# Performance work log

Hardware: AMD Instinct MI355X
Metric: run time of the kernel (lower is better)

Reference implementation:

```python
import jax, jax.numpy as jnp
import numpy as np

TEMP = 0.1        # Similarity temperature (nonzero -> cosine path)
PAD = -100.0      # padding value used by the torch module
EPS = 1e-8        # F.cosine_similarity default eps


def setup_inputs() -> dict:
    key = jax.random.key(0)
    k1, k2, k3 = jax.random.split(key, 3)
    B, S, D = 8, 4096, 1024
    sequence_output = jax.random.normal(k1, (B, S, D), dtype=jnp.float32)
    cls = jax.random.randint(k2, (B, S), 0, 2, dtype=jnp.int32)
    is_eop = jax.random.uniform(k3, (B, S)) < 0.25
    labels = jnp.where(is_eop, cls, -100).astype(jnp.int32)
    return {"sequence_output": sequence_output, "labels": labels}


def reference(sequence_output, labels):
    # sequence_output: [B, S, D]; labels: [B, S] with -100 = ignore
    B, S, D = sequence_output.shape
    mask = labels != -100                      # [B, S]
    cnt = mask.sum(axis=1)                     # [B] eop sentence count per example
    # Stable argsort brings masked (eop) positions to the front, preserving order
    order = jnp.argsort(jnp.logical_not(mask), axis=1, stable=True)  # [B, S]
    gathered = jnp.take_along_axis(sequence_output, order[..., None], axis=1)  # [B, S, D]
    glabels = jnp.take_along_axis(labels, order, axis=1)                        # [B, S]

    pos = jnp.arange(S)[None, :]               # [1, S]
    cnt_safe = jnp.maximum(cnt, 1)[:, None]    # avoid %0 for empty examples
    nxt = (pos + 1) % cnt_safe                 # [B, S] cyclic next-sentence index
    next_vec = jnp.take_along_axis(gathered, nxt[..., None], axis=1)  # [B, S, D]

    dot = jnp.sum(gathered * next_vec, axis=-1)                 # [B, S]
    nx = jnp.linalg.norm(gathered, axis=-1)
    ny = jnp.linalg.norm(next_vec, axis=-1)
    cos = dot / jnp.maximum(nx * ny, EPS) / TEMP                # cosine / temp

    valid = pos < cnt[:, None]                                  # [B, S]
    # Torch pads to the max eop count in the batch; we pad to S (static upper
    # bound) with the same -100 fill so the math on valid slots is identical.
    cos_out = jnp.where(valid, cos, PAD)
    lab_out = jnp.where(valid, glabels, -100)
    return cos_out, lab_out
```

## Files before the change

### kernel.cpp

```cpp
#include <hip/hip_runtime.h>

#define BB 8
#define SS 4096
#define DD 1024
#define TEMP 0.1f
#define PADV -100.0f
#define EPSV 1e-8f

__global__ __launch_bounds__(1024) void compact_kernel(const int* __restrict__ labels,
                                                       int2* __restrict__ desc,
                                                       float* __restrict__ out_cos,
                                                       float* __restrict__ out_lab) {
    int b = blockIdx.x;
    int t = threadIdx.x;
    int lane = t & 63, wave = t >> 6;

    __shared__ int pos[SS];
    __shared__ int wsum[16];

    int4 v = ((const int4*)(labels + b * SS))[t];
    int vals[4] = {v.x, v.y, v.z, v.w};
    int mycnt = (vals[0] != -100) + (vals[1] != -100) + (vals[2] != -100) + (vals[3] != -100);

    int scan = mycnt;
#pragma unroll
    for (int off = 1; off < 64; off <<= 1) {
        int n = __shfl_up(scan, off, 64);
        if (lane >= off) scan += n;
    }
    if (lane == 63) wsum[wave] = scan;
    __syncthreads();

    int wbase = 0, c = 0;
#pragma unroll
    for (int w = 0; w < 16; ++w) {
        int s = wsum[w];
        wbase += (w < wave) ? s : 0;
        c += s;
    }
    int o = wbase + scan - mycnt;

#pragma unroll
    for (int i = 0; i < 4; ++i) {
        if (vals[i] != -100) {
            pos[o]              = 4 * t + i;
            out_lab[b * SS + o] = (float)vals[i];
            ++o;
        }
    }
#pragma unroll
    for (int i = 0; i < 4; ++i) {
        int s = 4 * t + i;
        if (s >= c) { out_lab[b * SS + s] = PADV; out_cos[b * SS + s] = PADV; }
    }
    __syncthreads();

    int2 d[4];
#pragma unroll
    for (int i = 0; i < 4; ++i) {
        int j = 4 * t + i;
        if (j < c) {
            int jn = (j + 1 == c) ? 0 : (j + 1);
            d[i].x = pos[j];
            d[i].y = pos[jn];
        } else {
            d[i].x = -1;
            d[i].y = -1;
        }
    }
    int4* dp = (int4*)(desc + (size_t)b * SS + 4 * t);
    dp[0] = make_int4(d[0].x, d[0].y, d[1].x, d[1].y);
    dp[1] = make_int4(d[2].x, d[2].y, d[3].x, d[3].y);
}

__global__ __launch_bounds__(256) void cos_kernel(const float* __restrict__ x,
                                                  const int2* __restrict__ desc,
                                                  float* __restrict__ out_cos) {
    int b    = blockIdx.y;
    int lane = threadIdx.x & 63;
    int wid  = threadIdx.x >> 6;
    int j0   = (blockIdx.x * 4 + wid) * 2;

    int4 D = *(const int4*)(desc + (size_t)b * SS + j0);
    if (D.x < 0) return;
    bool p1 = (D.z >= 0);
    int i0 = D.x, i1 = D.y;
    int i2 = p1 ? D.w : D.y;

    const float* xb = x + (size_t)b * SS * DD + (size_t)lane * 4;
    const float* pa = xb + (size_t)i0 * DD;
    const float* pb = xb + (size_t)i1 * DD;
    const float* pc = xb + (size_t)i2 * DD;

    float4 A[4], B[4], C[4];
#pragma unroll
    for (int q = 0; q < 4; ++q) {
        A[q] = *(const float4*)(pa + q * 256);
        B[q] = *(const float4*)(pb + q * 256);
        C[q] = *(const float4*)(pc + q * 256);
    }

    float na = 0.f, nb = 0.f, nc = 0.f, dab = 0.f, dbc = 0.f;
#pragma unroll
    for (int q = 0; q < 4; ++q) {
        na  += A[q].x*A[q].x + A[q].y*A[q].y + A[q].z*A[q].z + A[q].w*A[q].w;
        nb  += B[q].x*B[q].x + B[q].y*B[q].y + B[q].z*B[q].z + B[q].w*B[q].w;
        nc  += C[q].x*C[q].x + C[q].y*C[q].y + C[q].z*C[q].z + C[q].w*C[q].w;
        dab += A[q].x*B[q].x + A[q].y*B[q].y + A[q].z*B[q].z + A[q].w*B[q].w;
        dbc += B[q].x*C[q].x + B[q].y*C[q].y + B[q].z*C[q].z + B[q].w*C[q].w;
    }
#pragma unroll
    for (int off = 32; off; off >>= 1) {
        na  += __shfl_xor(na,  off, 64);
        nb  += __shfl_xor(nb,  off, 64);
        nc  += __shfl_xor(nc,  off, 64);
        dab += __shfl_xor(dab, off, 64);
        dbc += __shfl_xor(dbc, off, 64);
    }

    if (lane == 0) {
        float r0 = dab / fmaxf(sqrtf(na) * sqrtf(nb), EPSV) / TEMP;
        float* op = out_cos + b * SS + j0;
        if (p1) {
            float r1 = dbc / fmaxf(sqrtf(nb) * sqrtf(nc), EPSV) / TEMP;
            *(float2*)op = make_float2(r0, r1);
        } else {
            *op = r0;
        }
    }
}

extern "C" void kernel_launch(void* const* d_in, const int* in_sizes, int n_in,
                              void* d_out, int out_size, void* d_ws, size_t ws_size,
                              hipStream_t stream) {
    const float* seq    = (const float*)d_in[0];
    const int*   labels = (const int*)d_in[1];

    float* out_cos = (float*)d_out;
    float* out_lab = (float*)d_out + BB * SS;

    int2* desc = (int2*)d_ws;

    compact_kernel<<<BB, 1024, 0, stream>>>(labels, desc, out_cos, out_lab);

    dim3 grid(SS / 8, BB);
    cos_kernel<<<grid, 256, 0, stream>>>(seq, desc, out_cos);
}
```

Baseline: 16.51 us.

## Stage shared row vectors in LDS via direct global-to-LDS loads per block

Each block now handles 8 consecutive compacted positions and loads the 9 distinct rows they need into shared memory once, using the direct global_load_lds builtin. Waves then read their three rows from LDS instead of reloading overlapping rows from global memory. This removes the duplicate fetch of the boundary row shared by adjacent waves (12 row loads per block down to 9). In exchange it adds a block-wide barrier, 36KB of LDS per block that limits occupancy, and an extra LDS round trip.

Result: slower. 17.38 us (+5.3%).

```diff
diff --git a/kernel.cpp b/kernel.cpp
--- a/kernel.cpp
+++ b/kernel.cpp
@@ -6,6 +6,9 @@
 #define TEMP 0.1f
 #define PADV -100.0f
 #define EPSV 1e-8f
+
+typedef __attribute__((address_space(1))) const void GV;
+typedef __attribute__((address_space(3))) void LV;
 
 __global__ __launch_bounds__(1024) void compact_kernel(const int* __restrict__ labels,
                                                        int2* __restrict__ desc,
@@ -77,27 +80,60 @@
                                                   const int2* __restrict__ desc,
                                                   float* __restrict__ out_cos) {
     int b    = blockIdx.y;
-    int lane = threadIdx.x & 63;
-    int wid  = threadIdx.x >> 6;
-    int j0   = (blockIdx.x * 4 + wid) * 2;
+    int j0   = blockIdx.x * 8;
+    int t    = threadIdx.x;
+    int lane = t & 63, wid = t >> 6;
 
-    int4 D = *(const int4*)(desc + (size_t)b * SS + j0);
-    if (D.x < 0) return;
-    bool p1 = (D.z >= 0);
-    int i0 = D.x, i1 = D.y;
-    int i2 = p1 ? D.w : D.y;
+    __shared__ float buf[9 * 1024];
 
-    const float* xb = x + (size_t)b * SS * DD + (size_t)lane * 4;
-    const float* pa = xb + (size_t)i0 * DD;
-    const float* pb = xb + (size_t)i1 * DD;
-    const float* pc = xb + (size_t)i2 * DD;
+    const int2* dbase = desc + (size_t)b * SS + j0;
+    int4 d01 = *(const int4*)(dbase + 0);
+    if (d01.x < 0) return;
+    int4 d23 = *(const int4*)(dbase + 2);
+    int4 d45 = *(const int4*)(dbase + 4);
+    int4 d67 = *(const int4*)(dbase + 6);
+
+    int P0 = d01.x, P1 = d01.y, P2 = d01.w, P3 = d23.y, P4 = d23.w;
+    int P5 = d45.y, P6 = d45.w, P7 = d67.y, P8 = d67.w;
+
+    const float* xb = x + (size_t)b * SS * DD;
+
+#define STAGE_SLOT(S, PS)                                                      \
+    if ((PS) >= 0) {                                                           \
+        const float* g = xb + (size_t)(PS) * DD + lane * 4;                    \
+        _Pragma("unroll")                                                      \
+        for (int q = 0; q < 4; ++q) {                                          \
+            __builtin_amdgcn_global_load_lds((GV*)(g + q * 256),               \
+                                             (LV*)(&buf[((S) * 4 + q) * 256]), \
+                                             16, 0, 0);                        \
+        }                                                                      \
+    }
+
+    if (wid == 0)      { STAGE_SLOT(0, P0) STAGE_SLOT(1, P1) }
+    else if (wid == 1) { STAGE_SLOT(2, P2) STAGE_SLOT(3, P3) }
+    else if (wid == 2) { STAGE_SLOT(4, P4) STAGE_SLOT(5, P5) }
+    else               { STAGE_SLOT(6, P6) STAGE_SLOT(7, P7) STAGE_SLOT(8, P8) }
+#undef STAGE_SLOT
+
+    __syncthreads();
+
+    int vA, vB;
+    if (wid == 0)      { vA = d01.x; vB = d01.z; }
+    else if (wid == 1) { vA = d23.x; vB = d23.z; }
+    else if (wid == 2) { vA = d45.x; vB = d45.z; }
+    else               { vA = d67.x; vB = d67.z; }
+    if (vA < 0) return;
+
+    bool p1 = (vB >= 0);
+    const float4* lf = (const float4*)buf;
+    int sA = wid * 2;
 
     float4 A[4], B[4], C[4];
 #pragma unroll
     for (int q = 0; q < 4; ++q) {
-        A[q] = *(const float4*)(pa + q * 256);
-        B[q] = *(const float4*)(pb + q * 256);
-        C[q] = *(const float4*)(pc + q * 256);
+        A[q] = lf[(sA * 4 + q)       * 64 + lane];
+        B[q] = lf[((sA + 1) * 4 + q) * 64 + lane];
+        C[q] = lf[((sA + 2) * 4 + q) * 64 + lane];
     }
 
     float na = 0.f, nb = 0.f, nc = 0.f, dab = 0.f, dbc = 0.f;
@@ -119,8 +155,9 @@
     }
 
     if (lane == 0) {
+        int j = j0 + sA;
         float r0 = dab / fmaxf(sqrtf(na) * sqrtf(nb), EPSV) / TEMP;
-        float* op = out_cos + b * SS + j0;
+        float* op = out_cos + b * SS + j;
         if (p1) {
             float r1 = dbc / fmaxf(sqrtf(nb) * sqrtf(nc), EPSV) / TEMP;
             *(float2*)op = make_float2(r0, r1);
```
